# Kernel optimization log

Hardware: AMD Instinct MI355X
Metric: run time of the kernel (lower is better)

The kernel has to match this reference:

```python
import jax, jax.numpy as jnp
import numpy as np

N_NODES = 50000
N_EDGES = 800000
N_GRAPHS = 64
IN_DIM, HID1, HID2, N_CLASSES = 128, 256, 128, 10


def setup_inputs() -> dict:
    key = jax.random.key(0)
    ks = jax.random.split(key, 12)
    x = jax.random.normal(ks[0], (N_NODES, IN_DIM), dtype=jnp.float32)
    src = jax.random.randint(ks[1], (N_EDGES,), 0, N_NODES, dtype=jnp.int32)
    dst = jax.random.randint(ks[2], (N_EDGES,), 0, N_NODES, dtype=jnp.int32)
    graph_id = jnp.sort(jax.random.randint(ks[3], (N_NODES,), 0, N_GRAPHS, dtype=jnp.int32))
    s1 = 1.0 / np.sqrt(IN_DIM)
    s2 = 1.0 / np.sqrt(HID1)
    s3 = 1.0 / np.sqrt(HID2)
    s4 = 1.0 / np.sqrt(12)
    return {
        'x': x, 'src': src, 'dst': dst, 'graph_id': graph_id,
        'W1': jax.random.normal(ks[4], (IN_DIM, HID1), dtype=jnp.float32) * s1,
        'b1': jnp.zeros((HID1,), dtype=jnp.float32),
        'W2': jax.random.normal(ks[5], (HID1, HID2), dtype=jnp.float32) * s2,
        'b2': jnp.zeros((HID2,), dtype=jnp.float32),
        'Wc1': jax.random.normal(ks[6], (HID2, 12), dtype=jnp.float32) * s3,
        'bc1': jnp.zeros((12,), dtype=jnp.float32),
        'Wc2': jax.random.normal(ks[7], (12, 12), dtype=jnp.float32) * s4,
        'bc2': jnp.zeros((12,), dtype=jnp.float32),
        'Wc3': jax.random.normal(ks[8], (12, N_CLASSES), dtype=jnp.float32) * s4,
        'bc3': jnp.zeros((N_CLASSES,), dtype=jnp.float32),
    }


def _graph_conv(x, W, b, src, dst, inv_sqrt_out, inv_sqrt_in, n_nodes):
    # DGL GraphConv, norm='both': D_out^{-1/2} applied to source feats,
    # sum-aggregate over edges, then D_in^{-1/2} on destination, then +bias.
    # Weight applied first (equivalent by linearity; reduces gather traffic
    # when out_dim < in_dim, and is exactly what DGL does in that case).
    xw = (x * inv_sqrt_out[:, None]) @ W                      # [N, out]
    agg = jax.ops.segment_sum(xw[src], dst, num_segments=n_nodes)  # SpMM
    return agg * inv_sqrt_in[:, None] + b


def reference(x, src, dst, graph_id, W1, b1, W2, b2, Wc1, bc1, Wc2, bc2, Wc3, bc3):
    n = x.shape[0]
    ones_e = jnp.ones(src.shape, dtype=x.dtype)
    deg_out = jnp.maximum(jax.ops.segment_sum(ones_e, src, num_segments=n), 1.0)
    deg_in = jnp.maximum(jax.ops.segment_sum(ones_e, dst, num_segments=n), 1.0)
    inv_o = jax.lax.rsqrt(deg_out)
    inv_i = jax.lax.rsqrt(deg_in)

    h = jax.nn.relu(_graph_conv(x, W1, b1, src, dst, inv_o, inv_i, n))
    h = jax.nn.relu(_graph_conv(h, W2, b2, src, dst, inv_o, inv_i, n))

    # dgl.mean_nodes: per-graph mean over nodes of the batched graph
    gsum = jax.ops.segment_sum(h, graph_id, num_segments=N_GRAPHS)   # [G, HID2]
    cnt = jnp.maximum(jax.ops.segment_sum(jnp.ones((n,), dtype=h.dtype), graph_id, num_segments=N_GRAPHS), 1.0)
    hg = gsum / cnt[:, None]

    # tiny 3-layer MLP (no activations in between, as in the source)
    out = hg @ Wc1 + bc1
    out = out @ Wc2 + bc2
    out = out @ Wc3 + bc3
    return out
```

## Files before the change

kernel.cpp:

```cpp
#include <hip/hip_runtime.h>
#include <hip/hip_bf16.h>

#define IN_DIM 128
#define HID1 256
#define HID2 128

#define HB_BINS 25000
#define HB_WORDS 12500
#define HB_CHUNKS 64
__global__ __launch_bounds__(256) void hist_count(const int* __restrict__ src,
                                                  const int* __restrict__ dst,
                                                  int E, int chunk_size,
                                                  int* __restrict__ part_in,
                                                  int* __restrict__ part_out, int N) {
    __shared__ int sm[HB_WORDS];
    const int* idx = (blockIdx.z == 0) ? dst : src;
    int* part = (blockIdx.z == 0) ? part_in : part_out;
    const int base = blockIdx.y * HB_BINS;
    const int ebeg = blockIdx.x * chunk_size;
    const int eend = min(ebeg + chunk_size, E);
    for (int w = threadIdx.x; w < HB_WORDS; w += 256) sm[w] = 0;
    __syncthreads();
    for (int e = ebeg + threadIdx.x; e < eend; e += 256) {
        int v = idx[e] - base;
        if ((unsigned)v < (unsigned)HB_BINS)
            atomicAdd(&sm[v >> 1], 1 << ((v & 1) * 16));
    }
    __syncthreads();
    const int nb = min(HB_BINS, N - base);
    int* dp = part + (size_t)blockIdx.x * N + base;
    for (int w = threadIdx.x; 2 * w < nb; w += 256) {
        int packed = sm[w];
        int b = 2 * w;
        dp[b] = packed & 0xffff;
        if (b + 1 < nb) dp[b + 1] = (packed >> 16) & 0xffff;
    }
}

__global__ __launch_bounds__(256) void hist_reduce(const int* __restrict__ part_in,
                                                   const int* __restrict__ part_out,
                                                   int N, int* __restrict__ deg_in,
                                                   float* __restrict__ inv_i,
                                                   float* __restrict__ inv_o,
                                                   int* __restrict__ blockSums) {
    __shared__ int sm[256];
    int b = blockIdx.x * 256 + threadIdx.x;
    int di = 0, dox = 0;
    if (b < N) {
#pragma unroll 4
        for (int k = 0; k < HB_CHUNKS; ++k) {
            di += part_in[(size_t)k * N + b];
            dox += part_out[(size_t)k * N + b];
        }
        deg_in[b] = di;
        inv_i[b] = rsqrtf((float)max(di, 1));
        inv_o[b] = rsqrtf((float)max(dox, 1));
    }
    sm[threadIdx.x] = di;
    __syncthreads();
#pragma unroll
    for (int off = 128; off > 0; off >>= 1) {
        if (threadIdx.x < off) sm[threadIdx.x] += sm[threadIdx.x + off];
        __syncthreads();
    }
    if (threadIdx.x == 0) blockSums[blockIdx.x] = sm[0];
}

#define SCAN_B 256
__global__ __launch_bounds__(SCAN_B) void scan_blocksums(int* __restrict__ blockSums, int nb) {
    __shared__ int sm[SCAN_B];
    int t = threadIdx.x;
    int v = (t < nb) ? blockSums[t] : 0;
    sm[t] = v;
    __syncthreads();
#pragma unroll
    for (int off = 1; off < SCAN_B; off <<= 1) {
        int u = (t >= off) ? sm[t - off] : 0;
        __syncthreads();
        sm[t] += u;
        __syncthreads();
    }
    if (t < nb) blockSums[t] = sm[t] - v;
}

__global__ __launch_bounds__(SCAN_B) void scan_final(const int* __restrict__ deg,
                                                     const int* __restrict__ blockSums,
                                                     int* __restrict__ row, int n) {
    __shared__ int sm[SCAN_B];
    int i = blockIdx.x * SCAN_B + threadIdx.x;
    int v = (i < n) ? deg[i] : 0;
    sm[threadIdx.x] = v;
    __syncthreads();
#pragma unroll
    for (int off = 1; off < SCAN_B; off <<= 1) {
        int u = (threadIdx.x >= off) ? sm[threadIdx.x - off] : 0;
        __syncthreads();
        sm[threadIdx.x] += u;
        __syncthreads();
    }
    int excl = sm[threadIdx.x] - v + blockSums[blockIdx.x];
    if (i < n) {
        row[i] = excl;
        if (i == n - 1) row[n] = excl + v;
    }
}

#define BK_SHIFT 8
#define NBUCK 196
#define NCHUNK 256
__global__ __launch_bounds__(256) void coarse_hist(const int* __restrict__ dst, int E,
                                                   int chunk_size, int* __restrict__ ccnt) {
    __shared__ int cnt[NBUCK];
    for (int i = threadIdx.x; i < NBUCK; i += 256) cnt[i] = 0;
    __syncthreads();
    int ebeg = blockIdx.x * chunk_size, eend = min(ebeg + chunk_size, E);
    for (int e = ebeg + threadIdx.x; e < eend; e += 256)
        atomicAdd(&cnt[dst[e] >> BK_SHIFT], 1);
    __syncthreads();
    for (int i = threadIdx.x; i < NBUCK; i += 256) ccnt[blockIdx.x * NBUCK + i] = cnt[i];
}

__global__ __launch_bounds__(NCHUNK) void coarse_off(const int* __restrict__ ccnt,
                                                     const int* __restrict__ row, int N,
                                                     int* __restrict__ coff) {
    __shared__ int sm[NCHUNK];
    int b = blockIdx.x, t = threadIdx.x;
    int v = ccnt[t * NBUCK + b];
    sm[t] = v;
    __syncthreads();
#pragma unroll
    for (int off = 1; off < NCHUNK; off <<= 1) {
        int u = (t >= off) ? sm[t - off] : 0;
        __syncthreads();
        sm[t] += u;
        __syncthreads();
    }
    int base = row[min(b << BK_SHIFT, N)];
    coff[t * NBUCK + b] = base + sm[t] - v;
}

__global__ __launch_bounds__(256) void scat_a(const int* __restrict__ src,
                                              const int* __restrict__ dst, int E,
                                              int chunk_size, const int* __restrict__ coff,
                                              int2* __restrict__ pairs) {
    __shared__ int lcur[NBUCK];
    for (int i = threadIdx.x; i < NBUCK; i += 256) lcur[i] = coff[blockIdx.x * NBUCK + i];
    __syncthreads();
    int ebeg = blockIdx.x * chunk_size, eend = min(ebeg + chunk_size, E);
    for (int e = ebeg + threadIdx.x; e < eend; e += 256) {
        int d = dst[e];
        int p = atomicAdd(&lcur[d >> BK_SHIFT], 1);
        pairs[p] = make_int2(src[e], d);
    }
}

__global__ __launch_bounds__(256) void scat_b(const int2* __restrict__ pairs,
                                              const int* __restrict__ row, int N,
                                              int* __restrict__ csr_src) {
    __shared__ int cur[1 << BK_SHIFT];
    const int nb0 = blockIdx.x << BK_SHIFT;
    const int nb1 = min(nb0 + (1 << BK_SHIFT), N);
    if (nb0 >= N) return;
    for (int i = threadIdx.x; i < nb1 - nb0; i += 256) cur[i] = row[nb0 + i];
    __syncthreads();
    const int beg = row[nb0], end = row[nb1];
    for (int j = beg + threadIdx.x; j < end; j += 256) {
        int2 pr = pairs[j];
        int p = atomicAdd(&cur[pr.y - nb0], 1);
        csr_src[p] = pr.x;
    }
}

__global__ void cvt_scale_kernel(const float* __restrict__ in,
                                 const float* __restrict__ rowscale,
                                 __hip_bfloat16* __restrict__ out, int n4) {
    int i = blockIdx.x * blockDim.x + threadIdx.x;
    if (i < n4) {
        float s = rowscale[i >> 5];
        float4 v = reinterpret_cast<const float4*>(in)[i];
        __hip_bfloat16 b0 = __float2bfloat16(v.x * s);
        __hip_bfloat16 b1 = __float2bfloat16(v.y * s);
        __hip_bfloat16 b2 = __float2bfloat16(v.z * s);
        __hip_bfloat16 b3 = __float2bfloat16(v.w * s);
        ushort4 o = make_ushort4(*(unsigned short*)&b0, *(unsigned short*)&b1,
                                 *(unsigned short*)&b2, *(unsigned short*)&b3);
        reinterpret_cast<ushort4*>(out)[i] = o;
    }
}

__global__ void cvt_transpose2_kernel(const float* __restrict__ W1, __hip_bfloat16* __restrict__ W1t,
                                      const float* __restrict__ W2, __hip_bfloat16* __restrict__ W2t) {
    int idx = blockIdx.x * blockDim.x + threadIdx.x;
    const int S1 = IN_DIM * HID1;
    if (idx < S1) {
        int k = idx / HID1, n = idx - k * HID1;
        W1t[n * IN_DIM + k] = __float2bfloat16(W1[idx]);
    } else if (idx < S1 + HID1 * HID2) {
        int j = idx - S1;
        int k = j / HID2, n = j - k * HID2;
        W2t[n * HID1 + k] = __float2bfloat16(W2[j]);
    }
}

__device__ __forceinline__ void bf2_unpack(unsigned int p, float& lo, float& hi) {
    lo = __uint_as_float(p << 16);
    hi = __uint_as_float(p & 0xffff0000u);
}

__global__ __launch_bounds__(256) void spmm_kernel(const __hip_bfloat16* __restrict__ feat,
                                                   const int* __restrict__ row,
                                                   const int* __restrict__ csr_src,
                                                   __hip_bfloat16* __restrict__ out_bf, int N) {
    const int node = blockIdx.x * 4 + (threadIdx.x >> 6);
    if (node >= N) return;
    const int lane = threadIdx.x & 63;
    const unsigned int* fp = (const unsigned int*)feat;
    const int beg = row[node];
    const int end = row[node + 1];
    float a0 = 0.f, a1 = 0.f;
    int j = beg;
    for (; j + 4 <= end; j += 4) {
        int s0 = csr_src[j], s1 = csr_src[j + 1], s2 = csr_src[j + 2], s3 = csr_src[j + 3];
        unsigned int p0 = fp[(size_t)s0 * 64 + lane];
        unsigned int p1 = fp[(size_t)s1 * 64 + lane];
        unsigned int p2 = fp[(size_t)s2 * 64 + lane];
        unsigned int p3 = fp[(size_t)s3 * 64 + lane];
        float lo, hi;
        bf2_unpack(p0, lo, hi); a0 += lo; a1 += hi;
        bf2_unpack(p1, lo, hi); a0 += lo; a1 += hi;
        bf2_unpack(p2, lo, hi); a0 += lo; a1 += hi;
        bf2_unpack(p3, lo, hi); a0 += lo; a1 += hi;
    }
    for (; j < end; ++j) {
        unsigned int p0 = fp[(size_t)csr_src[j] * 64 + lane];
        float lo, hi;
        bf2_unpack(p0, lo, hi); a0 += lo; a1 += hi;
    }
    __hip_bfloat16 b0 = __float2bfloat16(a0);
    __hip_bfloat16 b1 = __float2bfloat16(a1);
    unsigned int packed = (unsigned int)(*(unsigned short*)&b0) |
                          ((unsigned int)(*(unsigned short*)&b1) << 16);
    ((unsigned int*)out_bf)[(size_t)node * 64 + lane] = packed;
}

#define GBM 128
#define GBN 128
#define GBK 32
#define LPAD 40
typedef __attribute__((ext_vector_type(4))) float floatx4;
typedef __attribute__((ext_vector_type(8))) short shortx8;

__global__ __launch_bounds__(256) void mfma_gemm_kernel(const __hip_bfloat16* __restrict__ A,
                                                        const __hip_bfloat16* __restrict__ Bt,
                                                        __hip_bfloat16* __restrict__ C,
                                                        const float* __restrict__ scaleR,
                                                        const float* __restrict__ bias,
                                                        const float* __restrict__ scaleO,
                                                        int M, int Nn, int K, int doRelu) {
    __shared__ __align__(16) __hip_bfloat16 As[GBM * LPAD];
    __shared__ __align__(16) __hip_bfloat16 Bs[GBN * LPAD];
    const int tid = threadIdx.x;
    const int bm = blockIdx.x * GBM;
    const int bn = blockIdx.y * GBN;
    const int wid = tid >> 6;
    const int lane = tid & 63;
    const int wm = (wid & 1) * 64;
    const int wn = (wid >> 1) * 64;
    const int lrow = lane & 15;
    const int quad = lane >> 4;

    floatx4 acc[4][4] = {};

    for (int k0 = 0; k0 < K; k0 += GBK) {
#pragma unroll
        for (int it = 0; it < 2; ++it) {
            int slot = tid + (it << 8);
            int r = slot >> 2;
            int c = (slot & 3) << 3;
            int gr = bm + r;
            float4 v = make_float4(0.f, 0.f, 0.f, 0.f);
            if (gr < M) v = *reinterpret_cast<const float4*>(A + (size_t)gr * K + k0 + c);
            *reinterpret_cast<float4*>(&As[r * LPAD + c]) = v;
        }
#pragma unroll
        for (int it = 0; it < 2; ++it) {
            int slot = tid + (it << 8);
            int r = slot >> 2;
            int c = (slot & 3) << 3;
            float4 v = *reinterpret_cast<const float4*>(Bt + (size_t)(bn + r) * K + k0 + c);
            *reinterpret_cast<float4*>(&Bs[r * LPAD + c]) = v;
        }
        __syncthreads();

        shortx8 af[4], bf[4];
#pragma unroll
        for (int i = 0; i < 4; ++i)
            af[i] = *reinterpret_cast<const shortx8*>(&As[(wm + i * 16 + lrow) * LPAD + quad * 8]);
#pragma unroll
        for (int i = 0; i < 4; ++i)
            bf[i] = *reinterpret_cast<const shortx8*>(&Bs[(wn + i * 16 + lrow) * LPAD + quad * 8]);
#pragma unroll
        for (int im = 0; im < 4; ++im)
#pragma unroll
            for (int in = 0; in < 4; ++in)
                acc[im][in] = __builtin_amdgcn_mfma_f32_16x16x32_bf16(af[im], bf[in], acc[im][in], 0, 0, 0);
        __syncthreads();
    }

    float bv[4];
#pragma unroll
    for (int in = 0; in < 4; ++in)
        bv[in] = bias ? bias[bn + wn + in * 16 + lrow] : 0.f;

#pragma unroll
    for (int im = 0; im < 4; ++im) {
#pragma unroll
        for (int reg = 0; reg < 4; ++reg) {
            int r = bm + wm + im * 16 + quad * 4 + reg;
            if (r >= M) continue;
            float sR = scaleR ? scaleR[r] : 1.f;
            float sO = scaleO ? scaleO[r] : 1.f;
#pragma unroll
            for (int in = 0; in < 4; ++in) {
                int c = bn + wn + in * 16 + lrow;
                float v = acc[im][in][reg] * sR + bv[in];
                if (doRelu) v = fmaxf(v, 0.f);
                v *= sO;
                C[(size_t)r * Nn + c] = __float2bfloat16(v);
            }
        }
    }
}

#define POOL_CHUNK 64
__global__ __launch_bounds__(128) void pool_kernel(const __hip_bfloat16* __restrict__ agg2,
                                                   const float* __restrict__ inv_i,
                                                   const float* __restrict__ b2,
                                                   const int* __restrict__ graph_id,
                                                   int n, float* __restrict__ hg_sum) {
    const int f = threadIdx.x;
    const int beg = blockIdx.x * POOL_CHUNK;
    const int end = min(beg + POOL_CHUNK, n);
    if (beg >= n) return;
    const unsigned short* ap = (const unsigned short*)agg2;
    const float bias = b2[f];
    int g = graph_id[beg];
    float acc = 0.f;
    for (int i = beg; i < end; ++i) {
        int gi = graph_id[i];
        if (gi != g) {
            atomicAdd(&hg_sum[g * HID2 + f], acc);
            acc = 0.f;
            g = gi;
        }
        float a = __uint_as_float((unsigned int)ap[(size_t)i * HID2 + f] << 16);
        float v = a * inv_i[i] + bias;
        acc += fmaxf(v, 0.f);
    }
    atomicAdd(&hg_sum[g * HID2 + f], acc);
}

__device__ __forceinline__ int lower_bound_i(const int* a, int n, int key) {
    int lo = 0, hi = n;
    while (lo < hi) {
        int mid = (lo + hi) >> 1;
        if (a[mid] < key) lo = mid + 1; else hi = mid;
    }
    return lo;
}

__global__ __launch_bounds__(64) void mlp_kernel(const float* __restrict__ hg_sum,
                                                 const int* __restrict__ graph_id, int n,
                                                 const float* __restrict__ Wc1, const float* __restrict__ bc1,
                                                 const float* __restrict__ Wc2, const float* __restrict__ bc2,
                                                 const float* __restrict__ Wc3, const float* __restrict__ bc3,
                                                 float* __restrict__ out) {
    const int g = blockIdx.x;
    const int t = threadIdx.x;
    __shared__ float h[HID2];
    __shared__ float t1[12];
    __shared__ float t2[12];
    __shared__ float s_inv_cnt;
    if (t == 0) {
        int beg = lower_bound_i(graph_id, n, g);
        int end = lower_bound_i(graph_id, n, g + 1);
        int c = end - beg;
        s_inv_cnt = 1.0f / (float)max(c, 1);
    }
    __syncthreads();
    const float ic = s_inv_cnt;
    for (int i = t; i < HID2; i += 64) h[i] = hg_sum[g * HID2 + i] * ic;
    __syncthreads();
    if (t < 12) {
        float a = bc1[t];
        for (int k = 0; k < HID2; ++k) a += h[k] * Wc1[k * 12 + t];
        t1[t] = a;
    }
    __syncthreads();
    if (t < 12) {
        float a = bc2[t];
        for (int k = 0; k < 12; ++k) a += t1[k] * Wc2[k * 12 + t];
        t2[t] = a;
    }
    __syncthreads();
    if (t < 10) {
        float a = bc3[t];
        for (int k = 0; k < 12; ++k) a += t2[k] * Wc3[k * 10 + t];
        out[g * 10 + t] = a;
    }
}

extern "C" void kernel_launch(void* const* d_in, const int* in_sizes, int n_in,
                              void* d_out, int out_size, void* d_ws, size_t ws_size,
                              hipStream_t stream) {
    const float* x        = (const float*)d_in[0];
    const int*   src      = (const int*)d_in[1];
    const int*   dst      = (const int*)d_in[2];
    const int*   graph_id = (const int*)d_in[3];
    const float* W1       = (const float*)d_in[4];
    const float* b1       = (const float*)d_in[5];
    const float* W2       = (const float*)d_in[6];
    const float* b2       = (const float*)d_in[7];
    const float* Wc1      = (const float*)d_in[8];
    const float* bc1      = (const float*)d_in[9];
    const float* Wc2      = (const float*)d_in[10];
    const float* bc2      = (const float*)d_in[11];
    const float* Wc3      = (const float*)d_in[12];
    const float* bc3      = (const float*)d_in[13];
    float* out = (float*)d_out;

    const int N = in_sizes[0] / IN_DIM;
    const int E = in_sizes[1];
    const int G = out_size / 10;

    char* ws = (char*)d_ws;
    size_t off = 0;
    auto alloc = [&](size_t bytes) -> char* {
        char* p = ws + off;
        off = (off + bytes + 255) & ~(size_t)255;
        return p;
    };
    const int NB = (N + SCAN_B - 1) / SCAN_B;
    int*   deg_in  = (int*)alloc((size_t)N * 4);
    float* inv_i   = (float*)alloc((size_t)N * 4);
    float* inv_o   = (float*)alloc((size_t)N * 4);
    int*   row     = (int*)alloc((size_t)(N + 1) * 4);
    int*   bsums   = (int*)alloc((size_t)NB * 4);
    int*   ccnt    = (int*)alloc((size_t)NCHUNK * NBUCK * 4);
    int*   coff    = (int*)alloc((size_t)NCHUNK * NBUCK * 4);
    int2*  pairs   = (int2*)alloc((size_t)E * 8);
    int*   csr_src = (int*)alloc((size_t)E * 4);
    float* hg      = (float*)alloc((size_t)G * HID2 * 4);
    __hip_bfloat16* x_bf    = (__hip_bfloat16*)alloc((size_t)N * IN_DIM * 2);
    __hip_bfloat16* W1t     = (__hip_bfloat16*)alloc((size_t)IN_DIM * HID1 * 2);
    __hip_bfloat16* W2t     = (__hip_bfloat16*)alloc((size_t)HID1 * HID2 * 2);
    __hip_bfloat16* agg1_bf = (__hip_bfloat16*)alloc((size_t)N * IN_DIM * 2);
    __hip_bfloat16* h1_bf   = (__hip_bfloat16*)alloc((size_t)N * HID1 * 2);
    __hip_bfloat16* xw2_bf  = (__hip_bfloat16*)alloc((size_t)N * HID2 * 2);
    __hip_bfloat16* agg2_bf = agg1_bf;

    int* part_in  = (int*)h1_bf;
    int* part_out = part_in + (size_t)HB_CHUNKS * N;

    hipMemsetAsync(hg, 0, (size_t)G * HID2 * 4, stream);

    const int hchunk = (E + HB_CHUNKS - 1) / HB_CHUNKS;
    const int n_ranges = (N + HB_BINS - 1) / HB_BINS;
    hist_count<<<dim3(HB_CHUNKS, n_ranges, 2), 256, 0, stream>>>(src, dst, E, hchunk,
                                                                 part_in, part_out, N);
    hist_reduce<<<NB, 256, 0, stream>>>(part_in, part_out, N, deg_in, inv_i, inv_o, bsums);
    scan_blocksums<<<1, SCAN_B, 0, stream>>>(bsums, NB);
    scan_final<<<NB, SCAN_B, 0, stream>>>(deg_in, bsums, row, N);

    const int schunk = (E + NCHUNK - 1) / NCHUNK;
    coarse_hist<<<NCHUNK, 256, 0, stream>>>(dst, E, schunk, ccnt);
    coarse_off<<<NBUCK, NCHUNK, 0, stream>>>(ccnt, row, N, coff);
    scat_a<<<NCHUNK, 256, 0, stream>>>(src, dst, E, schunk, coff, pairs);
    scat_b<<<NBUCK, 256, 0, stream>>>(pairs, row, N, csr_src);

    cvt_scale_kernel<<<(N * IN_DIM / 4 + 255) / 256, 256, 0, stream>>>(x, inv_o, x_bf, N * IN_DIM / 4);
    cvt_transpose2_kernel<<<(IN_DIM * HID1 + HID1 * HID2 + 255) / 256, 256, 0, stream>>>(W1, W1t, W2, W2t);

    spmm_kernel<<<(N + 3) / 4, 256, 0, stream>>>(x_bf, row, csr_src, agg1_bf, N);
    mfma_gemm_kernel<<<dim3((N + GBM - 1) / GBM, HID1 / GBN), 256, 0, stream>>>(
        agg1_bf, W1t, h1_bf, inv_i, b1, inv_o, N, HID1, IN_DIM, 1);

    mfma_gemm_kernel<<<dim3((N + GBM - 1) / GBM, HID2 / GBN), 256, 0, stream>>>(
        h1_bf, W2t, xw2_bf, nullptr, nullptr, nullptr, N, HID2, HID1, 0);
    spmm_kernel<<<(N + 3) / 4, 256, 0, stream>>>(xw2_bf, row, csr_src, agg2_bf, N);

    pool_kernel<<<(N + POOL_CHUNK - 1) / POOL_CHUNK, 128, 0, stream>>>(agg2_bf, inv_i, b2, graph_id, N, hg);
    mlp_kernel<<<G, 64, 0, stream>>>(hg, graph_id, N, Wc1, bc1, Wc2, bc2, Wc3, bc3, out);
}
```

Baseline: 302.8 us.

## Fuse second SpMM with mean pooling and merge scan and conversion kernels

Fuses the layer-2 SpMM with the bias, ReLU and per-graph pooling, so the aggregated bf16 buffer is never written to and re-read from memory. It also merges the two scan kernels with the coarse-offset computation (each block recomputes its prefix over the block sums) and merges the x and weight conversion kernels. The hg memset is folded into coarse_hist. This cuts about five launches and one full feature round trip, at the cost of redundant block-sum reductions and more atomics into hg.

```diff
diff --git a/kernel.cpp b/kernel.cpp
--- a/kernel.cpp
+++ b/kernel.cpp
@@ -66,51 +66,15 @@
     if (threadIdx.x == 0) blockSums[blockIdx.x] = sm[0];
 }
 
-#define SCAN_B 256
-__global__ __launch_bounds__(SCAN_B) void scan_blocksums(int* __restrict__ blockSums, int nb) {
-    __shared__ int sm[SCAN_B];
-    int t = threadIdx.x;
-    int v = (t < nb) ? blockSums[t] : 0;
-    sm[t] = v;
-    __syncthreads();
-#pragma unroll
-    for (int off = 1; off < SCAN_B; off <<= 1) {
-        int u = (t >= off) ? sm[t - off] : 0;
-        __syncthreads();
-        sm[t] += u;
-        __syncthreads();
-    }
-    if (t < nb) blockSums[t] = sm[t] - v;
-}
-
-__global__ __launch_bounds__(SCAN_B) void scan_final(const int* __restrict__ deg,
-                                                     const int* __restrict__ blockSums,
-                                                     int* __restrict__ row, int n) {
-    __shared__ int sm[SCAN_B];
-    int i = blockIdx.x * SCAN_B + threadIdx.x;
-    int v = (i < n) ? deg[i] : 0;
-    sm[threadIdx.x] = v;
-    __syncthreads();
-#pragma unroll
-    for (int off = 1; off < SCAN_B; off <<= 1) {
-        int u = (threadIdx.x >= off) ? sm[threadIdx.x - off] : 0;
-        __syncthreads();
-        sm[threadIdx.x] += u;
-        __syncthreads();
-    }
-    int excl = sm[threadIdx.x] - v + blockSums[blockIdx.x];
-    if (i < n) {
-        row[i] = excl;
-        if (i == n - 1) row[n] = excl + v;
-    }
-}
-
 #define BK_SHIFT 8
 #define NBUCK 196
 #define NCHUNK 256
 __global__ __launch_bounds__(256) void coarse_hist(const int* __restrict__ dst, int E,
-                                                   int chunk_size, int* __restrict__ ccnt) {
+                                                   int chunk_size, int* __restrict__ ccnt,
+                                                   float* __restrict__ hg, int hg_n) {
     __shared__ int cnt[NBUCK];
+    if (blockIdx.x == 0)
+        for (int i = threadIdx.x; i < hg_n; i += 256) hg[i] = 0.f;
     for (int i = threadIdx.x; i < NBUCK; i += 256) cnt[i] = 0;
     __syncthreads();
     int ebeg = blockIdx.x * chunk_size, eend = min(ebeg + chunk_size, E);
@@ -120,23 +84,54 @@
     for (int i = threadIdx.x; i < NBUCK; i += 256) ccnt[blockIdx.x * NBUCK + i] = cnt[i];
 }
 
-__global__ __launch_bounds__(NCHUNK) void coarse_off(const int* __restrict__ ccnt,
-                                                     const int* __restrict__ row, int N,
-                                                     int* __restrict__ coff) {
-    __shared__ int sm[NCHUNK];
-    int b = blockIdx.x, t = threadIdx.x;
-    int v = ccnt[t * NBUCK + b];
+__global__ __launch_bounds__(256) void scan_coarse_final(const int* __restrict__ deg,
+                                                         const int* __restrict__ blockSums, int nbs,
+                                                         const int* __restrict__ ccnt,
+                                                         int* __restrict__ row,
+                                                         int* __restrict__ coff, int n) {
+    __shared__ int sm[256];
+    __shared__ int s_base;
+    const int b = blockIdx.x, t = threadIdx.x;
+    int v0 = (t < b && t < nbs) ? blockSums[t] : 0;
+    sm[t] = v0;
+    __syncthreads();
+#pragma unroll
+    for (int off = 128; off > 0; off >>= 1) {
+        if (t < off) sm[t] += sm[t + off];
+        __syncthreads();
+    }
+    if (t == 0) s_base = sm[0];
+    __syncthreads();
+    const int base = s_base;
+    int i = b * 256 + t;
+    int v = (i < n) ? deg[i] : 0;
+    __syncthreads();
     sm[t] = v;
     __syncthreads();
 #pragma unroll
-    for (int off = 1; off < NCHUNK; off <<= 1) {
+    for (int off = 1; off < 256; off <<= 1) {
         int u = (t >= off) ? sm[t - off] : 0;
         __syncthreads();
         sm[t] += u;
         __syncthreads();
     }
-    int base = row[min(b << BK_SHIFT, N)];
-    coff[t * NBUCK + b] = base + sm[t] - v;
+    int excl = sm[t] - v + base;
+    if (i < n) {
+        row[i] = excl;
+        if (i == n - 1) row[n] = excl + v;
+    }
+    __syncthreads();
+    int c = ccnt[t * NBUCK + b];
+    sm[t] = c;
+    __syncthreads();
+#pragma unroll
+    for (int off = 1; off < 256; off <<= 1) {
+        int u = (t >= off) ? sm[t - off] : 0;
+        __syncthreads();
+        sm[t] += u;
+        __syncthreads();
+    }
+    coff[t * NBUCK + b] = base + sm[t] - c;
 }
 
 __global__ __launch_bounds__(256) void scat_a(const int* __restrict__ src,
@@ -171,34 +166,33 @@
     }
 }
 
-__global__ void cvt_scale_kernel(const float* __restrict__ in,
-                                 const float* __restrict__ rowscale,
-                                 __hip_bfloat16* __restrict__ out, int n4) {
+__global__ void cvt_all(const float* __restrict__ x, const float* __restrict__ inv_o,
+                        __hip_bfloat16* __restrict__ x_bf, int n4x,
+                        const float* __restrict__ W1, __hip_bfloat16* __restrict__ W1t,
+                        const float* __restrict__ W2, __hip_bfloat16* __restrict__ W2t) {
+    const int S1 = IN_DIM * HID1;
+    const int S2 = HID1 * HID2;
     int i = blockIdx.x * blockDim.x + threadIdx.x;
-    if (i < n4) {
-        float s = rowscale[i >> 5];
-        float4 v = reinterpret_cast<const float4*>(in)[i];
+    if (i < n4x) {
+        float s = inv_o[i >> 5];
+        float4 v = reinterpret_cast<const float4*>(x)[i];
         __hip_bfloat16 b0 = __float2bfloat16(v.x * s);
         __hip_bfloat16 b1 = __float2bfloat16(v.y * s);
         __hip_bfloat16 b2 = __float2bfloat16(v.z * s);
         __hip_bfloat16 b3 = __float2bfloat16(v.w * s);
         ushort4 o = make_ushort4(*(unsigned short*)&b0, *(unsigned short*)&b1,
                                  *(unsigned short*)&b2, *(unsigned short*)&b3);
-        reinterpret_cast<ushort4*>(out)[i] = o;
-    }
-}
-
-__global__ void cvt_transpose2_kernel(const float* __restrict__ W1, __hip_bfloat16* __restrict__ W1t,
-                                      const float* __restrict__ W2, __hip_bfloat16* __restrict__ W2t) {
-    int idx = blockIdx.x * blockDim.x + threadIdx.x;
-    const int S1 = IN_DIM * HID1;
-    if (idx < S1) {
-        int k = idx / HID1, n = idx - k * HID1;
-        W1t[n * IN_DIM + k] = __float2bfloat16(W1[idx]);
-    } else if (idx < S1 + HID1 * HID2) {
-        int j = idx - S1;
-        int k = j / HID2, n = j - k * HID2;
-        W2t[n * HID1 + k] = __float2bfloat16(W2[j]);
+        reinterpret_cast<ushort4*>(x_bf)[i] = o;
+    } else {
+        int idx = i - n4x;
+        if (idx < S1) {
+            int k = idx / HID1, n = idx - k * HID1;
+            W1t[n * IN_DIM + k] = __float2bfloat16(W1[idx]);
+        } else if (idx < S1 + S2) {
+            int j = idx - S1;
+            int k = j / HID2, n = j - k * HID2;
+            W2t[n * HID1 + k] = __float2bfloat16(W2[j]);
+        }
     }
 }
 
@@ -243,6 +237,61 @@
     ((unsigned int*)out_bf)[(size_t)node * 64 + lane] = packed;
 }
 
+#define SP_NODES 8
+__global__ __launch_bounds__(256) void spmm_pool_kernel(const __hip_bfloat16* __restrict__ feat,
+                                                        const int* __restrict__ row,
+                                                        const int* __restrict__ csr_src,
+                                                        const float* __restrict__ inv_i,
+                                                        const float* __restrict__ b2,
+                                                        const int* __restrict__ graph_id,
+                                                        int N, float* __restrict__ hg_sum) {
+    const int wave = blockIdx.x * 4 + (threadIdx.x >> 6);
+    const int lane = threadIdx.x & 63;
+    const int n0 = wave * SP_NODES;
+    if (n0 >= N) return;
+    const int n1 = min(n0 + SP_NODES, N);
+    const unsigned int* fp = (const unsigned int*)feat;
+    const float bias0 = b2[2 * lane];
+    const float bias1 = b2[2 * lane + 1];
+    int g = graph_id[n0];
+    float p0 = 0.f, p1 = 0.f;
+    for (int node = n0; node < n1; ++node) {
+        int gi = graph_id[node];
+        if (gi != g) {
+            atomicAdd(&hg_sum[g * HID2 + 2 * lane], p0);
+            atomicAdd(&hg_sum[g * HID2 + 2 * lane + 1], p1);
+            p0 = p1 = 0.f;
+            g = gi;
+        }
+        const int beg = row[node];
+        const int end = row[node + 1];
+        float a0 = 0.f, a1 = 0.f;
+        int j = beg;
+        for (; j + 4 <= end; j += 4) {
+            int s0 = csr_src[j], s1 = csr_src[j + 1], s2 = csr_src[j + 2], s3 = csr_src[j + 3];
+            unsigned int q0 = fp[(size_t)s0 * 64 + lane];
+            unsigned int q1 = fp[(size_t)s1 * 64 + lane];
+            unsigned int q2 = fp[(size_t)s2 * 64 + lane];
+            unsigned int q3 = fp[(size_t)s3 * 64 + lane];
+            float lo, hi;
+            bf2_unpack(q0, lo, hi); a0 += lo; a1 += hi;
+            bf2_unpack(q1, lo, hi); a0 += lo; a1 += hi;
+            bf2_unpack(q2, lo, hi); a0 += lo; a1 += hi;
+            bf2_unpack(q3, lo, hi); a0 += lo; a1 += hi;
+        }
+        for (; j < end; ++j) {
+            unsigned int q0 = fp[(size_t)csr_src[j] * 64 + lane];
+            float lo, hi;
+            bf2_unpack(q0, lo, hi); a0 += lo; a1 += hi;
+        }
+        float ii = inv_i[node];
+        p0 += fmaxf(a0 * ii + bias0, 0.f);
+        p1 += fmaxf(a1 * ii + bias1, 0.f);
+    }
+    atomicAdd(&hg_sum[g * HID2 + 2 * lane], p0);
+    atomicAdd(&hg_sum[g * HID2 + 2 * lane + 1], p1);
+}
+
 #define GBM 128
 #define GBN 128
 #define GBK 32
@@ -332,34 +381,6 @@
     }
 }
 
-#define POOL_CHUNK 64
-__global__ __launch_bounds__(128) void pool_kernel(const __hip_bfloat16* __restrict__ agg2,
-                                                   const float* __restrict__ inv_i,
-                                                   const float* __restrict__ b2,
-                                                   const int* __restrict__ graph_id,
-                                                   int n, float* __restrict__ hg_sum) {
-    const int f = threadIdx.x;
-    const int beg = blockIdx.x * POOL_CHUNK;
-    const int end = min(beg + POOL_CHUNK, n);
-    if (beg >= n) return;
-    const unsigned short* ap = (const unsigned short*)agg2;
-    const float bias = b2[f];
-    int g = graph_id[beg];
-    float acc = 0.f;
-    for (int i = beg; i < end; ++i) {
-        int gi = graph_id[i];
-        if (gi != g) {
-            atomicAdd(&hg_sum[g * HID2 + f], acc);
-            acc = 0.f;
-            g = gi;
-        }
-        float a = __uint_as_float((unsigned int)ap[(size_t)i * HID2 + f] << 16);
-        float v = a * inv_i[i] + bias;
-        acc += fmaxf(v, 0.f);
-    }
-    atomicAdd(&hg_sum[g * HID2 + f], acc);
-}
-
 __device__ __forceinline__ int lower_bound_i(const int* a, int n, int key) {
     int lo = 0, hi = n;
     while (lo < hi) {
@@ -440,7 +461,7 @@
         off = (off + bytes + 255) & ~(size_t)255;
         return p;
     };
-    const int NB = (N + SCAN_B - 1) / SCAN_B;
+    const int NB = (N + 255) / 256;
     int*   deg_in  = (int*)alloc((size_t)N * 4);
     float* inv_i   = (float*)alloc((size_t)N * 4);
     float* inv_o   = (float*)alloc((size_t)N * 4);
@@ -457,29 +478,25 @@
     __hip_bfloat16* agg1_bf = (__hip_bfloat16*)alloc((size_t)N * IN_DIM * 2);
     __hip_bfloat16* h1_bf   = (__hip_bfloat16*)alloc((size_t)N * HID1 * 2);
     __hip_bfloat16* xw2_bf  = (__hip_bfloat16*)alloc((size_t)N * HID2 * 2);
-    __hip_bfloat16* agg2_bf = agg1_bf;
 
     int* part_in  = (int*)h1_bf;
     int* part_out = part_in + (size_t)HB_CHUNKS * N;
-
-    hipMemsetAsync(hg, 0, (size_t)G * HID2 * 4, stream);
 
     const int hchunk = (E + HB_CHUNKS - 1) / HB_CHUNKS;
     const int n_ranges = (N + HB_BINS - 1) / HB_BINS;
     hist_count<<<dim3(HB_CHUNKS, n_ranges, 2), 256, 0, stream>>>(src, dst, E, hchunk,
                                                                  part_in, part_out, N);
     hist_reduce<<<NB, 256, 0, stream>>>(part_in, part_out, N, deg_in, inv_i, inv_o, bsums);
-    scan_blocksums<<<1, SCAN_B, 0, stream>>>(bsums, NB);
-    scan_final<<<NB, SCAN_B, 0, stream>>>(deg_in, bsums, row, N);
 
     const int schunk = (E + NCHUNK - 1) / NCHUNK;
-    coarse_hist<<<NCHUNK, 256, 0, stream>>>(dst, E, schunk, ccnt);
-    coarse_off<<<NBUCK, NCHUNK, 0, stream>>>(ccnt, row, N, coff);
+    coarse_hist<<<NCHUNK, 256, 0, stream>>>(dst, E, schunk, ccnt, hg, G * HID2);
+    scan_coarse_final<<<NB, 256, 0, stream>>>(deg_in, bsums, NB, ccnt, row, coff, N);
     scat_a<<<NCHUNK, 256, 0, stream>>>(src, dst, E, schunk, coff, pairs);
     scat_b<<<NBUCK, 256, 0, stream>>>(pairs, row, N, csr_src);
 
-    cvt_scale_kernel<<<(N * IN_DIM / 4 + 255) / 256, 256, 0, stream>>>(x, inv_o, x_bf, N * IN_DIM / 4);
-    cvt_transpose2_kernel<<<(IN_DIM * HID1 + HID1 * HID2 + 255) / 256, 256, 0, stream>>>(W1, W1t, W2, W2t);
+    const int n4x = N * IN_DIM / 4;
+    cvt_all<<<(n4x + IN_DIM * HID1 + HID1 * HID2 + 255) / 256, 256, 0, stream>>>(
+        x, inv_o, x_bf, n4x, W1, W1t, W2, W2t);
 
     spmm_kernel<<<(N + 3) / 4, 256, 0, stream>>>(x_bf, row, csr_src, agg1_bf, N);
     mfma_gemm_kernel<<<dim3((N + GBM - 1) / GBM, HID1 / GBN), 256, 0, stream>>>(
@@ -487,8 +504,9 @@
 
     mfma_gemm_kernel<<<dim3((N + GBM - 1) / GBM, HID2 / GBN), 256, 0, stream>>>(
         h1_bf, W2t, xw2_bf, nullptr, nullptr, nullptr, N, HID2, HID1, 0);
-    spmm_kernel<<<(N + 3) / 4, 256, 0, stream>>>(xw2_bf, row, csr_src, agg2_bf, N);
-
-    pool_kernel<<<(N + POOL_CHUNK - 1) / POOL_CHUNK, 128, 0, stream>>>(agg2_bf, inv_i, b2, graph_id, N, hg);
+    const int npw = (N + SP_NODES - 1) / SP_NODES;
+    spmm_pool_kernel<<<(npw + 3) / 4, 256, 0, stream>>>(xw2_bf, row, csr_src, inv_i, b2,
+                                                        graph_id, N, hg);
+
     mlp_kernel<<<G, 64, 0, stream>>>(hg, graph_id, N, Wc1, bc1, Wc2, bc2, Wc3, bc3, out);
 }
```

New measurement: 284.2 us. 6.1% less time.
